# Performance work log

Hardware: AMD Instinct MI355X
Metric: run time of the kernel (lower is better)

The kernel has to match this reference:

```python
import math
import jax, jax.numpy as jnp
import numpy as np

N_NODES = 200000          # len(tree)
HIDDEN = 1024             # args.hidden_dim
SINGLE_DIM = HIDDEN // 2  # lower/upper halves of the circle embedding
TREE_HEIGHT = 8           # path length (root-to-leaf)
BATCH = 2048              # positive pairs per step
N_NEG = 8                 # args.negative_sample_size
CIRCLE_MARGIN = 1.0       # args.circle_margin
SCR = 2.0 * math.pi       # single_circle_range


def setup_inputs() -> dict:
    key = jax.random.key(0)
    k1, k2, k3 = jax.random.split(key, 3)
    node_embedding = jax.random.normal(k1, (N_NODES, HIDDEN), dtype=jnp.float32)
    pos_path = jax.random.randint(k2, (BATCH, 2, TREE_HEIGHT), 0, N_NODES, dtype=jnp.int32)
    neg_path = jax.random.randint(k3, (BATCH, N_NEG, TREE_HEIGHT), 0, N_NODES, dtype=jnp.int32)
    return {"node_embedding": node_embedding, "pos_path": pos_path, "neg_path": neg_path}


def _inter_size(p1, p2):
    # |set(path1) & set(path2)| assuming distinct ids within a path.
    # p1: [..., P], p2: [..., P] -> [...]
    return (p1[..., :, None] == p2[..., None, :]).any(-1).sum(-1)


def _calc_dist(emb, p1, p2, diff):
    # emb: [V, H]; p1, p2: [..., P] int; diff: [...] float
    d = emb[p1] - emb[p2]                       # [..., P, H]
    low, high = d[..., :SINGLE_DIM], d[..., SINGLE_DIM:]
    dist = (0.5 * (low + high)).sum(-2)         # [..., SINGLE_DIM]
    return dist + (diff - 1.0)[..., None] * SCR


def reference(node_embedding, pos_path, neg_path):
    p1 = pos_path[:, 0]                          # [B, P]
    p2 = pos_path[:, 1]                          # [B, P]
    # calc_dist clamps diff to >= 1; calc_diff (used for k) does NOT.
    diff_pos = jnp.maximum(TREE_HEIGHT - _inter_size(p1, p2), 1).astype(jnp.float32)
    pos_dist = _calc_dist(node_embedding, p1, p2, diff_pos)          # [B, SD]

    diff_neg_raw = (TREE_HEIGHT - _inter_size(p1[:, None, :], neg_path)).astype(jnp.float32)  # [B, N]
    k = diff_neg_raw - 1.0                                            # unclamped, per source
    diff_neg = jnp.maximum(diff_neg_raw, 1.0)
    neg_dist = _calc_dist(node_embedding, p1[:, None, :], neg_path, diff_neg)  # [B, N, SD]

    tmp = k[..., None] * CIRCLE_MARGIN * SCR + pos_dist[:, None, :] - neg_dist  # [B, N, SD]
    tmp_p = jnp.maximum(tmp, 0.0)
    punish = jnp.sqrt((tmp_p * tmp_p).sum(-1)).sum()   # sum of per-(b,n) L2 norms
    return punish.reshape(1)
```

## Files before the change

kernel.cpp:

```cpp
#include <hip/hip_runtime.h>

constexpr int   TH    = 8;
constexpr int   NNEG  = 8;
constexpr int   HID4  = 256;
constexpr int   FOLD4 = 128;
constexpr float SCR_F = 6.2831853071795864769f;

__global__ __launch_bounds__(256)
void flag_zero(int* __restrict__ flags, int n)
{
    for (int i = blockIdx.x * 256 + threadIdx.x; i < n; i += gridDim.x * 256)
        flags[i] = 0;
}

__global__ __launch_bounds__(256)
void flag_set(const int* __restrict__ pos_path,
              const int* __restrict__ neg_path,
              int* __restrict__ flags, int batch)
{
    const int tid = blockIdx.x * 256 + threadIdx.x;
    const int np2 = batch * TH;
    const int tot = np2 + batch * NNEG * TH;
    if (tid >= tot) return;
    int r;
    if (tid < np2) {
        const int b = tid / TH, h = tid % TH;
        r = pos_path[b * 2 * TH + TH + h];
    } else {
        r = neg_path[tid - np2];
    }
    flags[r] = 1;
}

__global__ __launch_bounds__(256)
void fold_kernel(const float* __restrict__ emb,
                 const int*   __restrict__ flags,
                 float*       __restrict__ folded,
                 int n_nodes)
{
    const int lane = threadIdx.x & 63;
    const int wave = blockIdx.x * 4 + (threadIdx.x >> 6);
    const int nwaves = gridDim.x * 4;

    const float4* __restrict__ embv = (const float4*)emb;
    float4* __restrict__ fv = (float4*)folded;

    for (int r = wave; r < n_nodes; r += nwaves) {
        if (!flags[r]) continue;
        const float4* row = embv + (long)r * HID4;
        const float4 a0 = row[lane];
        const float4 a1 = row[64 + lane];
        const float4 a2 = row[128 + lane];
        const float4 a3 = row[192 + lane];
        float4 o0, o1;
        o0.x = a0.x + a2.x; o0.y = a0.y + a2.y;
        o0.z = a0.z + a2.z; o0.w = a0.w + a2.w;
        o1.x = a1.x + a3.x; o1.y = a1.y + a3.y;
        o1.z = a1.z + a3.z; o1.w = a1.w + a3.w;
        fv[(long)r * FOLD4 + lane]      = o0;
        fv[(long)r * FOLD4 + 64 + lane] = o1;
    }
}

__global__ __launch_bounds__(64, 2)
void prep_kernel(const float* __restrict__ folded,
                 const int*   __restrict__ pos_path,
                 const int*   __restrict__ neg_path,
                 float*       __restrict__ sp2_out,
                 float*       __restrict__ C_out)
{
    const int b = blockIdx.x;
    const int l = threadIdx.x;

    if (l < NNEG) {
        int p1v[TH], p2v[TH];
#pragma unroll
        for (int i = 0; i < TH; i++) {
            p1v[i] = pos_path[b * 2 * TH + i];
            p2v[i] = pos_path[b * 2 * TH + TH + i];
        }
        int inter_pos = 0;
#pragma unroll
        for (int i = 0; i < TH; i++) {
            bool f = false;
#pragma unroll
            for (int j = 0; j < TH; j++) f = f || (p1v[i] == p2v[j]);
            inter_pos += f ? 1 : 0;
        }
        const float diff_pos = fmaxf((float)(TH - inter_pos), 1.0f);

        const int n = l;
        int negj[TH];
#pragma unroll
        for (int j = 0; j < TH; j++)
            negj[j] = neg_path[(b * NNEG + n) * TH + j];

        int inter_n = 0;
#pragma unroll
        for (int i = 0; i < TH; i++) {
            bool f = false;
#pragma unroll
            for (int j = 0; j < TH; j++) f = f || (p1v[i] == negj[j]);
            inter_n += f ? 1 : 0;
        }
        const int raw = TH - inter_n;
        C_out[b * NNEG + n] = (diff_pos - 1.0f - (raw == 0 ? 1.0f : 0.0f)) * SCR_F;
    }

    const float4* __restrict__ fv = (const float4*)folded;
    float4 s0 = {0.f, 0.f, 0.f, 0.f};
    float4 s1 = {0.f, 0.f, 0.f, 0.f};
#pragma unroll
    for (int h = 0; h < TH; h++) {
        const int r = pos_path[b * 2 * TH + TH + h];
        const float4* row = fv + (long)r * FOLD4;
        const float4 f0 = row[l];
        const float4 f1 = row[64 + l];
        s0.x += f0.x; s0.y += f0.y; s0.z += f0.z; s0.w += f0.w;
        s1.x += f1.x; s1.y += f1.y; s1.z += f1.z; s1.w += f1.w;
    }
    float4* sp2v = (float4*)sp2_out;
    sp2v[(long)b * FOLD4 + l]      = s0;
    sp2v[(long)b * FOLD4 + 64 + l] = s1;
}

__global__ __launch_bounds__(64, 2)
void neg_kernel(const float* __restrict__ folded,
                const int*   __restrict__ neg_path,
                const float* __restrict__ sp2_in,
                const float* __restrict__ C_in,
                float*       __restrict__ partial,
                int batch)
{
    const int bn = blockIdx.x;
    const int b  = bn % batch;
    const int n  = bn / batch;
    const int l  = threadIdx.x;
    const int idx = b * NNEG + n;

    const int4* __restrict__ npv = (const int4*)(neg_path + (long)idx * TH);
    const int4 nlo = npv[0];
    const int4 nhi = npv[1];
    const int ridx[TH] = {nlo.x, nlo.y, nlo.z, nlo.w, nhi.x, nhi.y, nhi.z, nhi.w};
    const float c = C_in[idx];

    const float4* __restrict__ fv = (const float4*)folded;
    float4 s0 = {0.f, 0.f, 0.f, 0.f};
    float4 s1 = {0.f, 0.f, 0.f, 0.f};
#pragma unroll
    for (int h = 0; h < TH; h++) {
        const float4* row = fv + (long)ridx[h] * FOLD4;
        const float4 f0 = row[l];
        const float4 f1 = row[64 + l];
        s0.x += f0.x; s0.y += f0.y; s0.z += f0.z; s0.w += f0.w;
        s1.x += f1.x; s1.y += f1.y; s1.z += f1.z; s1.w += f1.w;
    }

    const float4* sp2v = (const float4*)sp2_in;
    const float4 p0 = sp2v[(long)b * FOLD4 + l];
    const float4 p1 = sp2v[(long)b * FOLD4 + 64 + l];

    float v, a = 0.f;
    v = c + 0.5f * (s0.x - p0.x); v = fmaxf(v, 0.f); a += v * v;
    v = c + 0.5f * (s0.y - p0.y); v = fmaxf(v, 0.f); a += v * v;
    v = c + 0.5f * (s0.z - p0.z); v = fmaxf(v, 0.f); a += v * v;
    v = c + 0.5f * (s0.w - p0.w); v = fmaxf(v, 0.f); a += v * v;
    v = c + 0.5f * (s1.x - p1.x); v = fmaxf(v, 0.f); a += v * v;
    v = c + 0.5f * (s1.y - p1.y); v = fmaxf(v, 0.f); a += v * v;
    v = c + 0.5f * (s1.z - p1.z); v = fmaxf(v, 0.f); a += v * v;
    v = c + 0.5f * (s1.w - p1.w); v = fmaxf(v, 0.f); a += v * v;

#pragma unroll
    for (int off = 32; off > 0; off >>= 1) {
        a += __shfl_down(a, off, 64);
    }
    if (l == 0) partial[idx] = sqrtf(a);
}

__global__ __launch_bounds__(1024)
void reduce_kernel(const float* __restrict__ partial, int nval,
                   float* __restrict__ out)
{
    const int t = threadIdx.x;
    float s = 0.f;
    for (int i = t; i < nval; i += 1024) s += partial[i];

#pragma unroll
    for (int off = 32; off > 0; off >>= 1) {
        s += __shfl_down(s, off, 64);
    }
    __shared__ float s_red[16];
    const int lane = t & 63;
    const int wid  = t >> 6;
    if (lane == 0) s_red[wid] = s;
    __syncthreads();
    if (t == 0) {
        float tot = 0.f;
#pragma unroll
        for (int w = 0; w < 16; w++) tot += s_red[w];
        out[0] = tot;
    }
}

extern "C" void kernel_launch(void* const* d_in, const int* in_sizes, int n_in,
                              void* d_out, int out_size, void* d_ws, size_t ws_size,
                              hipStream_t stream) {
    const float* emb      = (const float*)d_in[0];
    const int*   pos_path = (const int*)d_in[1];
    const int*   neg_path = (const int*)d_in[2];
    float*       out      = (float*)d_out;

    const int BATCH   = in_sizes[1] / (2 * TH);
    const int N_NODES = in_sizes[0] / 1024;

    float* folded  = (float*)d_ws;
    int*   flags   = (int*)(folded + (size_t)N_NODES * 512);
    float* sp2     = (float*)(flags + N_NODES);
    float* Cb      = sp2 + (size_t)BATCH * 512;
    float* partial = Cb  + (size_t)BATCH * NNEG;

    const int refs = BATCH * (TH + NNEG * TH);

    flag_zero<<<512, 256, 0, stream>>>(flags, N_NODES);
    flag_set<<<(refs + 255) / 256, 256, 0, stream>>>(pos_path, neg_path,
                                                     flags, BATCH);
    fold_kernel<<<2048, 256, 0, stream>>>(emb, flags, folded, N_NODES);
    prep_kernel<<<BATCH, 64, 0, stream>>>(folded, pos_path, neg_path, sp2, Cb);
    neg_kernel<<<BATCH * NNEG, 64, 0, stream>>>(folded, neg_path, sp2, Cb,
                                                partial, BATCH);
    reduce_kernel<<<1, 1024, 0, stream>>>(partial, BATCH * NNEG, out);
}
```

Measured before the change: 1.042 ms.

## Scatter folded rows to per-reference contiguous buffer via inverted index

Builds an inverted index (per-row atomic cursor plus up to 32 entries) mapping each referenced embedding row to its path slots. The fold kernel then writes each folded row straight into every slot that uses it, so the later kernels read contiguous memory instead of gathering randomly. This turns random gathers into streaming reads at the cost of more writes (one folded row per reference, about 147K rows of 2KB) and atomics. A row referenced more than 32 times would be dropped silently.

```diff
diff --git a/kernel.cpp b/kernel.cpp
--- a/kernel.cpp
+++ b/kernel.cpp
@@ -4,49 +4,58 @@
 constexpr int   NNEG  = 8;
 constexpr int   HID4  = 256;
 constexpr int   FOLD4 = 128;
+constexpr int   CAP   = 32;
 constexpr float SCR_F = 6.2831853071795864769f;
 
 __global__ __launch_bounds__(256)
-void flag_zero(int* __restrict__ flags, int n)
+void cursor_zero(int* __restrict__ cursor, int n)
 {
     for (int i = blockIdx.x * 256 + threadIdx.x; i < n; i += gridDim.x * 256)
-        flags[i] = 0;
+        cursor[i] = 0;
 }
 
 __global__ __launch_bounds__(256)
-void flag_set(const int* __restrict__ pos_path,
+void idx_fill(const int* __restrict__ pos_path,
               const int* __restrict__ neg_path,
-              int* __restrict__ flags, int batch)
-{
-    const int tid = blockIdx.x * 256 + threadIdx.x;
+              int* __restrict__ cursor,
+              int* __restrict__ entries,
+              int batch)
+{
+    const int e   = blockIdx.x * 256 + threadIdx.x;
     const int np2 = batch * TH;
     const int tot = np2 + batch * NNEG * TH;
-    if (tid >= tot) return;
-    int r;
-    if (tid < np2) {
-        const int b = tid / TH, h = tid % TH;
-        r = pos_path[b * 2 * TH + TH + h];
+    if (e >= tot) return;
+    int row, chunk;
+    if (e < np2) {
+        const int b = e >> 3, h = e & 7;
+        row   = pos_path[b * 2 * TH + TH + h];
+        chunk = batch * NNEG * TH + e;
     } else {
-        r = neg_path[tid - np2];
-    }
-    flags[r] = 1;
+        const int en = e - np2;
+        row   = neg_path[en];
+        chunk = en;
+    }
+    const int j = atomicAdd(&cursor[row], 1);
+    if (j < CAP) entries[(row << 5) + j] = chunk;
 }
 
 __global__ __launch_bounds__(256)
-void fold_kernel(const float* __restrict__ emb,
-                 const int*   __restrict__ flags,
-                 float*       __restrict__ folded,
+void push_kernel(const float* __restrict__ emb,
+                 const int*   __restrict__ cursor,
+                 const int*   __restrict__ entries,
+                 float*       __restrict__ dest,
                  int n_nodes)
 {
     const int lane = threadIdx.x & 63;
     const int wave = blockIdx.x * 4 + (threadIdx.x >> 6);
-    const int nwaves = gridDim.x * 4;
+    const int nw   = gridDim.x * 4;
 
     const float4* __restrict__ embv = (const float4*)emb;
-    float4* __restrict__ fv = (float4*)folded;
-
-    for (int r = wave; r < n_nodes; r += nwaves) {
-        if (!flags[r]) continue;
+    float4* __restrict__ dv = (float4*)dest;
+
+    for (int r = wave; r < n_nodes; r += nw) {
+        const int c = cursor[r];
+        if (c == 0) continue;
         const float4* row = embv + (long)r * HID4;
         const float4 a0 = row[lane];
         const float4 a1 = row[64 + lane];
@@ -57,17 +66,23 @@
         o0.z = a0.z + a2.z; o0.w = a0.w + a2.w;
         o1.x = a1.x + a3.x; o1.y = a1.y + a3.y;
         o1.z = a1.z + a3.z; o1.w = a1.w + a3.w;
-        fv[(long)r * FOLD4 + lane]      = o0;
-        fv[(long)r * FOLD4 + 64 + lane] = o1;
-    }
-}
-
-__global__ __launch_bounds__(64, 2)
-void prep_kernel(const float* __restrict__ folded,
-                 const int*   __restrict__ pos_path,
-                 const int*   __restrict__ neg_path,
-                 float*       __restrict__ sp2_out,
-                 float*       __restrict__ C_out)
+        const int cc = (c < CAP) ? c : CAP;
+        for (int k = 0; k < cc; ++k) {
+            const int chunk = entries[(r << 5) + k];
+            float4* d = dv + (long)chunk * FOLD4;
+            d[lane]      = o0;
+            d[64 + lane] = o1;
+        }
+    }
+}
+
+__global__ __launch_bounds__(64)
+void sp2_kernel(const float* __restrict__ dest,
+                const int*   __restrict__ pos_path,
+                const int*   __restrict__ neg_path,
+                float*       __restrict__ sp2_out,
+                float*       __restrict__ C_out,
+                int batch)
 {
     const int b = blockIdx.x;
     const int l = threadIdx.x;
@@ -107,15 +122,14 @@
         C_out[b * NNEG + n] = (diff_pos - 1.0f - (raw == 0 ? 1.0f : 0.0f)) * SCR_F;
     }
 
-    const float4* __restrict__ fv = (const float4*)folded;
+    const float4* __restrict__ dv =
+        (const float4*)dest + (long)(batch * NNEG * TH + b * TH) * FOLD4;
     float4 s0 = {0.f, 0.f, 0.f, 0.f};
     float4 s1 = {0.f, 0.f, 0.f, 0.f};
 #pragma unroll
     for (int h = 0; h < TH; h++) {
-        const int r = pos_path[b * 2 * TH + TH + h];
-        const float4* row = fv + (long)r * FOLD4;
-        const float4 f0 = row[l];
-        const float4 f1 = row[64 + l];
+        const float4 f0 = dv[h * FOLD4 + l];
+        const float4 f1 = dv[h * FOLD4 + 64 + l];
         s0.x += f0.x; s0.y += f0.y; s0.z += f0.z; s0.w += f0.w;
         s1.x += f1.x; s1.y += f1.y; s1.z += f1.z; s1.w += f1.w;
     }
@@ -124,34 +138,23 @@
     sp2v[(long)b * FOLD4 + 64 + l] = s1;
 }
 
-__global__ __launch_bounds__(64, 2)
-void neg_kernel(const float* __restrict__ folded,
-                const int*   __restrict__ neg_path,
-                const float* __restrict__ sp2_in,
-                const float* __restrict__ C_in,
-                float*       __restrict__ partial,
-                int batch)
-{
-    const int bn = blockIdx.x;
-    const int b  = bn % batch;
-    const int n  = bn / batch;
-    const int l  = threadIdx.x;
-    const int idx = b * NNEG + n;
-
-    const int4* __restrict__ npv = (const int4*)(neg_path + (long)idx * TH);
-    const int4 nlo = npv[0];
-    const int4 nhi = npv[1];
-    const int ridx[TH] = {nlo.x, nlo.y, nlo.z, nlo.w, nhi.x, nhi.y, nhi.z, nhi.w};
-    const float c = C_in[idx];
-
-    const float4* __restrict__ fv = (const float4*)folded;
+__global__ __launch_bounds__(64)
+void neg2_kernel(const float* __restrict__ dest,
+                 const float* __restrict__ sp2_in,
+                 const float* __restrict__ C_in,
+                 float*       __restrict__ partial)
+{
+    const int s = blockIdx.x;
+    const int l = threadIdx.x;
+    const int b = s >> 3;
+
+    const float4* __restrict__ dv = (const float4*)dest + (long)s * TH * FOLD4;
     float4 s0 = {0.f, 0.f, 0.f, 0.f};
     float4 s1 = {0.f, 0.f, 0.f, 0.f};
 #pragma unroll
     for (int h = 0; h < TH; h++) {
-        const float4* row = fv + (long)ridx[h] * FOLD4;
-        const float4 f0 = row[l];
-        const float4 f1 = row[64 + l];
+        const float4 f0 = dv[h * FOLD4 + l];
+        const float4 f1 = dv[h * FOLD4 + 64 + l];
         s0.x += f0.x; s0.y += f0.y; s0.z += f0.z; s0.w += f0.w;
         s1.x += f1.x; s1.y += f1.y; s1.z += f1.z; s1.w += f1.w;
     }
@@ -159,6 +162,7 @@
     const float4* sp2v = (const float4*)sp2_in;
     const float4 p0 = sp2v[(long)b * FOLD4 + l];
     const float4 p1 = sp2v[(long)b * FOLD4 + 64 + l];
+    const float c = C_in[s];
 
     float v, a = 0.f;
     v = c + 0.5f * (s0.x - p0.x); v = fmaxf(v, 0.f); a += v * v;
@@ -174,7 +178,7 @@
     for (int off = 32; off > 0; off >>= 1) {
         a += __shfl_down(a, off, 64);
     }
-    if (l == 0) partial[idx] = sqrtf(a);
+    if (l == 0) partial[s] = sqrtf(a);
 }
 
 __global__ __launch_bounds__(1024)
@@ -210,23 +214,24 @@
     const int*   neg_path = (const int*)d_in[2];
     float*       out      = (float*)d_out;
 
-    const int BATCH   = in_sizes[1] / (2 * TH);
-    const int N_NODES = in_sizes[0] / 1024;
-
-    float* folded  = (float*)d_ws;
-    int*   flags   = (int*)(folded + (size_t)N_NODES * 512);
-    float* sp2     = (float*)(flags + N_NODES);
+    const int BATCH    = in_sizes[1] / (2 * TH);
+    const int N_NODES  = in_sizes[0] / 1024;
+    const int N_CHUNKS = BATCH * (NNEG * TH + TH);
+    const int N_REFS   = N_CHUNKS;
+
+    float* dest    = (float*)d_ws;
+    float* sp2     = dest + (size_t)N_CHUNKS * 512;
     float* Cb      = sp2 + (size_t)BATCH * 512;
     float* partial = Cb  + (size_t)BATCH * NNEG;
-
-    const int refs = BATCH * (TH + NNEG * TH);
-
-    flag_zero<<<512, 256, 0, stream>>>(flags, N_NODES);
-    flag_set<<<(refs + 255) / 256, 256, 0, stream>>>(pos_path, neg_path,
-                                                     flags, BATCH);
-    fold_kernel<<<2048, 256, 0, stream>>>(emb, flags, folded, N_NODES);
-    prep_kernel<<<BATCH, 64, 0, stream>>>(folded, pos_path, neg_path, sp2, Cb);
-    neg_kernel<<<BATCH * NNEG, 64, 0, stream>>>(folded, neg_path, sp2, Cb,
-                                                partial, BATCH);
+    int*   cursor  = (int*)(partial + (size_t)BATCH * NNEG);
+    int*   entries = cursor + N_NODES;
+
+    cursor_zero<<<512, 256, 0, stream>>>(cursor, N_NODES);
+    idx_fill<<<(N_REFS + 255) / 256, 256, 0, stream>>>(pos_path, neg_path,
+                                                       cursor, entries, BATCH);
+    push_kernel<<<4096, 256, 0, stream>>>(emb, cursor, entries, dest, N_NODES);
+    sp2_kernel<<<BATCH, 64, 0, stream>>>(dest, pos_path, neg_path, sp2, Cb,
+                                         BATCH);
+    neg2_kernel<<<BATCH * NNEG, 64, 0, stream>>>(dest, sp2, Cb, partial);
     reduce_kernel<<<1, 1024, 0, stream>>>(partial, BATCH * NNEG, out);
 }
```

New measurement: 1.101 ms. 5.6% more time.
